# Kernel optimization log

Hardware: AMD Instinct MI355X
Metric: run time of the kernel (lower is better)

The kernel has to match this reference:

```python
import jax, jax.numpy as jnp
import numpy as np

# Mamba config (HF defaults for hidden_size=256)
VOCAB = 4096
H = 256          # hidden_size
I = 512          # intermediate_size = 2*H
N = 16           # state_size
R = 16           # time_step_rank = ceil(H/16)
K = 4            # conv_kernel
NUM_LAYERS = 4
B, L = 4, 1024
EPS = 1e-5


def _rmsnorm(x, w):
    return x * jax.lax.rsqrt(jnp.mean(x * x, axis=-1, keepdims=True) + EPS) * w


def setup_inputs() -> dict:
    key = jax.random.key(0)
    ks = jax.random.split(key, 20)
    s = 0.02
    Lyr = NUM_LAYERS
    inp = {
        'input_ids': jax.random.randint(ks[0], (B, L), 0, VOCAB),
        'lengths': jax.random.randint(ks[1], (B,), 1, L + 1),
        'embed': jax.random.normal(ks[2], (VOCAB, H)) * s,
        'norm_w': jnp.ones((Lyr, H)),
        'in_proj_w': jax.random.normal(ks[3], (Lyr, 2 * I, H)) * s,
        'conv_w': jax.random.normal(ks[4], (Lyr, I, K)) * s,
        'conv_b': jnp.zeros((Lyr, I)),
        'x_proj_w': jax.random.normal(ks[5], (Lyr, R + 2 * N, I)) * s,
        'dt_proj_w': jax.random.normal(ks[6], (Lyr, I, R)) * s,
        'dt_proj_b': jax.random.normal(ks[7], (Lyr, I)) * 0.5 - 4.0,
        'A_log': jnp.log(jnp.broadcast_to(jnp.arange(1, N + 1, dtype=jnp.float32), (Lyr, I, N))),
        'D': jnp.ones((Lyr, I)),
        'out_proj_w': jax.random.normal(ks[8], (Lyr, H, I)) * s,
        'final_norm_w': jnp.ones((H,)),
        'head_w1': jax.random.normal(ks[9], (H // 4, H)) * s,
        'head_b1': jnp.zeros((H // 4,)),
        'head_w2': jax.random.normal(ks[10], (1, H // 4)) * s,
        'head_b2': jnp.zeros((1,)),
    }
    return inp


def _mixer(x, in_proj_w, conv_w, conv_b, x_proj_w, dt_proj_w, dt_proj_b, A_log, D_, out_proj_w):
    b, l, _ = x.shape
    proj = x @ in_proj_w.T                      # (b,l,2I)
    xs, gate = proj[..., :I], proj[..., I:]
    # depthwise causal conv1d (kernel K, left pad K-1)
    xp = jnp.pad(xs, ((0, 0), (K - 1, 0), (0, 0)))
    conv = sum(xp[:, k:k + l, :] * conv_w[:, k] for k in range(K))
    xs = jax.nn.silu(conv + conv_b)             # (b,l,I)
    ssm = xs @ x_proj_w.T                       # (b,l,R+2N)
    dt_r, Bmat, Cmat = ssm[..., :R], ssm[..., R:R + N], ssm[..., R + N:]
    dt = jax.nn.softplus(dt_r @ dt_proj_w.T + dt_proj_b)   # (b,l,I)
    A = -jnp.exp(A_log)                         # (I,N)
    dA = jnp.exp(dt[..., None] * A)             # (b,l,I,N)
    dBu = (dt * xs)[..., None] * Bmat[:, :, None, :]        # (b,l,I,N)

    def step(state, inputs):
        a_t, bu_t, c_t = inputs                 # (b,I,N),(b,I,N),(b,N)
        state = a_t * state + bu_t
        y = jnp.einsum('bdn,bn->bd', state, c_t)
        return state, y

    state0 = jnp.zeros((b, I, N), dtype=x.dtype)
    _, ys = jax.lax.scan(step, state0, (dA.transpose(1, 0, 2, 3),
                                        dBu.transpose(1, 0, 2, 3),
                                        Cmat.transpose(1, 0, 2)))
    ys = ys.transpose(1, 0, 2)                  # (b,l,I)
    y = (ys + xs * D_) * jax.nn.silu(gate)
    return y @ out_proj_w.T                     # (b,l,H)


def reference(input_ids, lengths, embed, norm_w, in_proj_w, conv_w, conv_b,
              x_proj_w, dt_proj_w, dt_proj_b, A_log, D, out_proj_w,
              final_norm_w, head_w1, head_b1, head_w2, head_b2):
    h = embed[input_ids]                        # (B,L,H)
    for i in range(NUM_LAYERS):
        res = h
        x = _rmsnorm(h, norm_w[i])
        h = res + _mixer(x, in_proj_w[i], conv_w[i], conv_b[i], x_proj_w[i],
                         dt_proj_w[i], dt_proj_b[i], A_log[i], D[i], out_proj_w[i])
    h = _rmsnorm(h, final_norm_w)
    pooled = h[jnp.arange(h.shape[0]), lengths - 1]         # (B,H)
    hd = jax.nn.gelu(pooled @ head_w1.T + head_b1, approximate=False)
    out = hd @ head_w2.T + head_b2
    return out.squeeze(-1)                      # (B,)
```

## Files before the change

### kernel.cpp

```cpp
#include <hip/hip_runtime.h>
#include <hip/hip_bf16.h>

#define HDIM 256
#define IDIM 512
#define NST 16
#define KCONV 4
#define LAYERS 4
#define BATCH 4
#define LSEQ 1024
#define TOK (BATCH * LSEQ)

typedef unsigned short u16;
typedef float f32x4 __attribute__((ext_vector_type(4)));
typedef short bf16x8 __attribute__((ext_vector_type(8)));

static __device__ __forceinline__ u16 f2bf(float f) {
    __hip_bfloat16 h = __float2bfloat16(f);
    return reinterpret_cast<u16&>(h);
}
static __device__ __forceinline__ float bf2f(u16 b) {
    return __builtin_bit_cast(float, (unsigned)b << 16);
}
static __device__ __forceinline__ float bfup(uint2 u, int j) {
    unsigned w = (j < 2) ? u.x : u.y;
    unsigned bits = (j & 1) ? (w & 0xffff0000u) : (w << 16);
    return __builtin_bit_cast(float, bits);
}

#define DPP_ROW_ADD(p, CTRL)                                                   \
    p += __builtin_bit_cast(float, __builtin_amdgcn_update_dpp(                \
             0, __builtin_bit_cast(int, p), CTRL, 0xf, 0xf, false))

__global__ __launch_bounds__(256) void embed_kernel(const int* __restrict__ ids,
                                                    const float* __restrict__ embed,
                                                    float* __restrict__ h) {
    int idx = blockIdx.x * 256 + threadIdx.x;
    if (idx < TOK * HDIM) {
        int tok = idx >> 8;
        int c = idx & (HDIM - 1);
        h[idx] = embed[ids[tok] * HDIM + c];
    }
}

__global__ __launch_bounds__(256) void cvt4_bf16_kernel(const float* __restrict__ s0, u16* __restrict__ d0,
                                                        const float* __restrict__ s1, u16* __restrict__ d1,
                                                        const float* __restrict__ s2, u16* __restrict__ d2,
                                                        const float* __restrict__ s3, u16* __restrict__ d3) {
    const float* in;
    u16* out;
    int base;
    int bid = blockIdx.x;
    if (bid < 1024)      { in = s0; out = d0; base = bid; }
    else if (bid < 1536) { in = s1; out = d1; base = bid - 1024; }
    else if (bid < 1632) { in = s2; out = d2; base = bid - 1536; }
    else                 { in = s3; out = d3; base = bid - 1632; }
    int j = (base * 256 + threadIdx.x) * 4;
    float4 v = *(const float4*)&in[j];
    unsigned lo = (unsigned)f2bf(v.x) | ((unsigned)f2bf(v.y) << 16);
    unsigned hi = (unsigned)f2bf(v.z) | ((unsigned)f2bf(v.w) << 16);
    *(uint2*)&out[j] = make_uint2(lo, hi);
}

__global__ __launch_bounds__(256) void rmsnorm_kernel(const float* __restrict__ h,
                                                      const float* __restrict__ w,
                                                      u16* __restrict__ xb) {
    int wid = threadIdx.x >> 6, lane = threadIdx.x & 63;
    int tok = blockIdx.x * 4 + wid;
    float4 v = *(const float4*)&h[(size_t)tok * HDIM + lane * 4];
    float s = v.x * v.x + v.y * v.y + v.z * v.z + v.w * v.w;
    #pragma unroll
    for (int m = 32; m >= 1; m >>= 1) s += __shfl_xor(s, m, 64);
    float rstd = rsqrtf(s * (1.0f / HDIM) + 1e-5f);
    float4 wv = *(const float4*)&w[lane * 4];
    unsigned lo = (unsigned)f2bf(v.x * rstd * wv.x) | ((unsigned)f2bf(v.y * rstd * wv.y) << 16);
    unsigned hi = (unsigned)f2bf(v.z * rstd * wv.z) | ((unsigned)f2bf(v.w * rstd * wv.w) << 16);
    *(uint2*)&xb[(size_t)tok * HDIM + lane * 4] = make_uint2(lo, hi);
}

__global__ __launch_bounds__(256) void gemm_bf16_kernel(const u16* __restrict__ A,
                                                        const u16* __restrict__ W,
                                                        u16* __restrict__ C,
                                                        int M, int N, int K) {
    const int BM = 128, BK = 32;
    __shared__ __align__(16) u16 Al[BM][BK + 8];
    __shared__ __align__(16) u16 Bl[BM][BK + 8];
    int m0 = blockIdx.y * BM, n0 = blockIdx.x * BM;
    int tid = threadIdx.x;
    int lane = tid & 63;
    int wid = tid >> 6;
    int wr = wid >> 1, wc = wid & 1;
    int r = lane & 15, g = lane >> 4;

    f32x4 acc[4][4] = {};

    int srow = tid & 127;
    const u16* src = (tid < 128) ? (A + (size_t)(m0 + srow) * K)
                                 : (W + (size_t)(n0 + srow) * K);
    u16* dstrow = (tid < 128) ? &Al[srow][0] : &Bl[srow][0];

    for (int k0 = 0; k0 < K; k0 += BK) {
        uint4 v0 = *(const uint4*)(src + k0);
        uint4 v1 = *(const uint4*)(src + k0 + 8);
        uint4 v2 = *(const uint4*)(src + k0 + 16);
        uint4 v3 = *(const uint4*)(src + k0 + 24);
        __syncthreads();
        *(uint4*)(dstrow)      = v0;
        *(uint4*)(dstrow + 8)  = v1;
        *(uint4*)(dstrow + 16) = v2;
        *(uint4*)(dstrow + 24) = v3;
        __syncthreads();

        bf16x8 af[4], bfr[4];
        #pragma unroll
        for (int f = 0; f < 4; ++f) {
            af[f]  = *(const bf16x8*)&Al[wr * 64 + f * 16 + r][g * 8];
            bfr[f] = *(const bf16x8*)&Bl[wc * 64 + f * 16 + r][g * 8];
        }
        #pragma unroll
        for (int fm = 0; fm < 4; ++fm)
            #pragma unroll
            for (int fn = 0; fn < 4; ++fn)
                acc[fm][fn] = __builtin_amdgcn_mfma_f32_16x16x32_bf16(
                    af[fm], bfr[fn], acc[fm][fn], 0, 0, 0);
    }

    #pragma unroll
    for (int fm = 0; fm < 4; ++fm) {
        #pragma unroll
        for (int fn = 0; fn < 4; ++fn) {
            int col = n0 + wc * 64 + fn * 16 + r;
            #pragma unroll
            for (int v = 0; v < 4; ++v) {
                int row = m0 + wr * 64 + fm * 16 + g * 4 + v;
                C[(size_t)row * N + col] = f2bf(acc[fm][fn][v]);
            }
        }
    }
}

__global__ __launch_bounds__(256) void outproj_norm_kernel(const u16* __restrict__ Y,
                                                           const u16* __restrict__ W,
                                                           const float* __restrict__ nw,
                                                           float* __restrict__ h,
                                                           u16* __restrict__ xb) {
    __shared__ float sH[16][260];
    int m0 = blockIdx.x * 16;
    int tid = threadIdx.x;
    int lane = tid & 63;
    int w = tid >> 6;
    int r = lane & 15, g = lane >> 4;

    f32x4 acc[4] = {};
    const u16* yrow  = Y + (size_t)(m0 + r) * 512 + g * 8;
    const u16* wbase = W + (size_t)(w * 64 + r) * 512 + g * 8;
    #pragma unroll
    for (int k0 = 0; k0 < 512; k0 += 32) {
        bf16x8 af = *(const bf16x8*)(yrow + k0);
        #pragma unroll
        for (int fn = 0; fn < 4; ++fn) {
            bf16x8 bfr = *(const bf16x8*)(wbase + (size_t)fn * 16 * 512 + k0);
            acc[fn] = __builtin_amdgcn_mfma_f32_16x16x32_bf16(af, bfr, acc[fn], 0, 0, 0);
        }
    }

    #pragma unroll
    for (int fn = 0; fn < 4; ++fn) {
        int col = w * 64 + fn * 16 + r;
        #pragma unroll
        for (int v = 0; v < 4; ++v) {
            int row = g * 4 + v;
            size_t off = (size_t)(m0 + row) * HDIM + col;
            float hv = h[off] + acc[fn][v];
            h[off] = hv;
            sH[row][col] = hv;
        }
    }
    __syncthreads();

    int row = tid >> 4, part = tid & 15;
    const float* sr = &sH[row][part * 16];
    float s = 0.f;
    #pragma unroll
    for (int j = 0; j < 16; ++j) s = fmaf(sr[j], sr[j], s);
    DPP_ROW_ADD(s, 0xB1);
    DPP_ROW_ADD(s, 0x4E);
    DPP_ROW_ADD(s, 0x141);
    DPP_ROW_ADD(s, 0x140);
    float rstd = rsqrtf(s * (1.0f / HDIM) + 1e-5f);
    const float* nwp = &nw[part * 16];
    unsigned pk[8];
    #pragma unroll
    for (int j = 0; j < 8; ++j) {
        u16 lo = f2bf(sr[2 * j]     * rstd * nwp[2 * j]);
        u16 hi = f2bf(sr[2 * j + 1] * rstd * nwp[2 * j + 1]);
        pk[j] = (unsigned)lo | ((unsigned)hi << 16);
    }
    u16* dst = xb + (size_t)(m0 + row) * HDIM + part * 16;
    *(uint4*)(dst)     = make_uint4(pk[0], pk[1], pk[2], pk[3]);
    *(uint4*)(dst + 8) = make_uint4(pk[4], pk[5], pk[6], pk[7]);
}

__global__ __launch_bounds__(512) void xproj_kernel(const u16* __restrict__ proj,
                                                    const float* __restrict__ cw,
                                                    const float* __restrict__ cb,
                                                    const u16* __restrict__ W,
                                                    const u16* __restrict__ dtw,
                                                    const float* __restrict__ dtb,
                                                    float* __restrict__ bc,
                                                    float* __restrict__ dtT,
                                                    u16* __restrict__ xs_T,
                                                    u16* __restrict__ gate_T) {
    __shared__ __align__(16) u16 xsL[16][520];
    __shared__ float sP[8][16][52];
    __shared__ float sT[16][52];
    int m0 = blockIdx.x * 16;
    int tid = threadIdx.x;
    int lane = tid & 63;
    int w = tid >> 6;
    int r = lane & 15, g = lane >> 4;
    int tl = m0 & (LSEQ - 1);

    {
        int ic = tid;
        const u16* pxs = proj + (size_t)m0 * 1024 + ic;
        float4 wq = *(const float4*)&cw[ic * 4];
        float bias = cb[ic];
        float a0 = (tl >= 3) ? bf2f(pxs[-3 * 1024]) : 0.f;
        float a1 = (tl >= 2) ? bf2f(pxs[-2 * 1024]) : 0.f;
        float a2 = (tl >= 1) ? bf2f(pxs[-1 * 1024]) : 0.f;
        unsigned xr[8], gr[8];
        #pragma unroll
        for (int t = 0; t < 16; ++t) {
            float a3 = bf2f(pxs[t * 1024]);
            float acc = bias;
            acc = fmaf(a0, wq.x, acc);
            acc = fmaf(a1, wq.y, acc);
            acc = fmaf(a2, wq.z, acc);
            acc = fmaf(a3, wq.w, acc);
            float xsv = acc / (1.f + __expf(-acc));
            u16 xb16 = f2bf(xsv);
            xsL[t][ic] = xb16;
            float gv = bf2f(pxs[t * 1024 + 512]);
            gv = gv / (1.f + __expf(-gv));
            u16 gb16 = f2bf(gv);
            if (t & 1) { xr[t >> 1] |= (unsigned)xb16 << 16; gr[t >> 1] |= (unsigned)gb16 << 16; }
            else       { xr[t >> 1] = xb16;                   gr[t >> 1] = gb16; }
            a0 = a1; a1 = a2; a2 = a3;
        }
        size_t trow = (size_t)ic * TOK + m0;
        *(uint4*)&xs_T[trow]       = make_uint4(xr[0], xr[1], xr[2], xr[3]);
        *(uint4*)&xs_T[trow + 8]   = make_uint4(xr[4], xr[5], xr[6], xr[7]);
        *(uint4*)&gate_T[trow]     = make_uint4(gr[0], gr[1], gr[2], gr[3]);
        *(uint4*)&gate_T[trow + 8] = make_uint4(gr[4], gr[5], gr[6], gr[7]);
    }
    __syncthreads();

    {
        f32x4 acc[3] = {};
        const u16* wbase = W + (size_t)r * 512 + w * 64 + g * 8;
        #pragma unroll
        for (int ks = 0; ks < 2; ++ks) {
            bf16x8 af = *(const bf16x8*)&xsL[r][w * 64 + ks * 32 + g * 8];
            #pragma unroll
            for (int fn = 0; fn < 3; ++fn) {
                bf16x8 bfr = *(const bf16x8*)(wbase + (size_t)fn * 16 * 512 + ks * 32);
                acc[fn] = __builtin_amdgcn_mfma_f32_16x16x32_bf16(af, bfr, acc[fn], 0, 0, 0);
            }
        }
        #pragma unroll
        for (int fn = 0; fn < 3; ++fn)
            #pragma unroll
            for (int v = 0; v < 4; ++v)
                sP[w][g * 4 + v][fn * 16 + r] = acc[fn][v];
    }
    __syncthreads();

    #pragma unroll
    for (int e = 0; e < 2; ++e) {
        int o = tid + e * 512;
        if (o < 768) {
            int row = o / 48, col = o - row * 48;
            float s = 0.f;
            #pragma unroll
            for (int p = 0; p < 8; ++p) s += sP[p][row][col];
            sT[row][col] = s;
        }
    }
    __syncthreads();

    {
        int l = tid;
        int group = l >> 7;
        int rem = l & 127;
        int side = rem >> 6;
        int nn = (rem >> 2) & 15;
        int tq = rem & 3;
        bc[(size_t)blockIdx.x * 512 + l] = sT[group * 4 + tq][16 + side * 16 + nn];
    }

    bf16x8 bv = {};
    if (g < 2) {
        #pragma unroll
        for (int j = 0; j < 8; ++j)
            bv[j] = (short)f2bf(sT[r][g * 8 + j]);
    }
    int mbase = w * 64;
    #pragma unroll
    for (int mf = 0; mf < 4; ++mf) {
        int mrow = mbase + mf * 16;
        bf16x8 av = {};
        if (g < 2) av = *(const bf16x8*)(dtw + (size_t)(mrow + r) * 16 + g * 8);
        f32x4 a2 = __builtin_amdgcn_mfma_f32_16x16x32_bf16(av, bv, f32x4{}, 0, 0, 0);
        float4 b4 = *(const float4*)&dtb[mrow + g * 4];
        #pragma unroll
        for (int v = 0; v < 4; ++v) {
            int i = mrow + g * 4 + v;
            float val = a2[v] + (&b4.x)[v];
            val = fmaxf(val, 0.f) + log1pf(__expf(-fabsf(val)));
            dtT[(size_t)i * TOK + m0 + r] = val;
        }
    }
}

__global__ __launch_bounds__(256, 4) void scan_kernel(const float* __restrict__ dt_T,
                                                      const u16* __restrict__ xs_T,
                                                      const u16* __restrict__ gate_T,
                                                      const float* __restrict__ bc,
                                                      const float* __restrict__ A_log,
                                                      const float* __restrict__ Dw,
                                                      u16* __restrict__ yb) {
    const int NC = 16;
    int n = threadIdx.x & 15;
    int c = threadIdx.x >> 4;

    int lin = (blockIdx.x & 7) * 256 + (blockIdx.x >> 3);
    int b = lin >> 9;
    int i = lin & (IDIM - 1);

    float A = -__expf(A_log[i * NST + n]);

    __shared__ float aprodS[NC][17];
    __shared__ float stendS[NC][17];
    __shared__ float incS[NC][17];

    int t0 = c * 64;
    size_t coff = (size_t)i * TOK + b * LSEQ + t0;
    const float4* dtp = (const float4*)(dt_T + coff);
    const uint2*  xsp = (const uint2*)(xs_T + coff);
    const u16*    xg  = xs_T + coff;
    const u16*    gg  = gate_T + coff;
    const float4* bp  = (const float4*)(bc + (size_t)(b * LSEQ + t0) * 32);

    float aprod = 1.f, st = 0.f;
    #pragma unroll
    for (int q = 0; q < 16; ++q) {
        float4 d4 = dtp[q];
        uint2  xu = xsp[q];
        float4 B4 = __builtin_bit_cast(float4, bp[q * 32 + n]);
        #pragma unroll
        for (int j = 0; j < 4; ++j) {
            float dtv = (&d4.x)[j];
            float dA  = __expf(dtv * A);
            aprod *= dA;
            st = fmaf(dA, st, dtv * bfup(xu, j) * (&B4.x)[j]);
        }
    }
    aprodS[c][n] = aprod;
    stendS[c][n] = st;
    __syncthreads();

    if (threadIdx.x < 16) {
        int nn = threadIdx.x;
        float carry = 0.f;
        for (int cc = 0; cc < NC; ++cc) {
            incS[cc][nn] = carry;
            carry = fmaf(aprodS[cc][nn], carry, stendS[cc][nn]);
        }
    }
    __syncthreads();

    st = incS[c][n];
    float Dv = Dw[i];
    u16* y_b = yb + ((size_t)b * LSEQ + t0) * IDIM + i;
    float yacc = 0.f;

    #pragma unroll 8
    for (int q = 0; q < 16; ++q) {
        float4 d4 = dtp[q];
        uint2  xu = xsp[q];
        float4 B4 = __builtin_bit_cast(float4, bp[q * 32 + n]);
        float4 C4 = __builtin_bit_cast(float4, bp[q * 32 + 16 + n]);
        #pragma unroll
        for (int j = 0; j < 4; ++j) {
            float dtv = (&d4.x)[j];
            float xv  = bfup(xu, j);
            float dA  = __expf(dtv * A);
            st = fmaf(dA, st, dtv * xv * (&B4.x)[j]);
            float py = st * (&C4.x)[j];
            DPP_ROW_ADD(py, 0xB1);
            DPP_ROW_ADD(py, 0x4E);
            DPP_ROW_ADD(py, 0x141);
            DPP_ROW_ADD(py, 0x140);
            yacc = (((q & 3) * 4 + j) == n) ? py : yacc;
        }
        if ((q & 3) == 3) {
            int base = (q - 3) * 4;
            float xvn = bf2f(xg[base + n]);
            float gvn = bf2f(gg[base + n]);
            float yv = fmaf(xvn, Dv, yacc) * gvn;
            y_b[(size_t)(base + n) * IDIM] = f2bf(yv);
        }
    }
}

__global__ __launch_bounds__(256) void head_kernel(const float* __restrict__ h,
                                                   const int* __restrict__ lengths,
                                                   const float* __restrict__ fw,
                                                   const float* __restrict__ w1,
                                                   const float* __restrict__ b1,
                                                   const float* __restrict__ w2,
                                                   const float* __restrict__ b2,
                                                   float* __restrict__ out) {
    int b = blockIdx.x;
    int c = threadIdx.x;
    int len = lengths[b];
    const float* row = h + ((size_t)b * LSEQ + (len - 1)) * HDIM;
    float v = row[c];
    float s = v * v;
    #pragma unroll
    for (int m = 32; m >= 1; m >>= 1) s += __shfl_xor(s, m, 64);
    __shared__ float ls[4];
    __shared__ float pooled[HDIM];
    __shared__ float hd[64];
    if ((c & 63) == 0) ls[c >> 6] = s;
    __syncthreads();
    float tot = ls[0] + ls[1] + ls[2] + ls[3];
    float rstd = rsqrtf(tot * (1.0f / HDIM) + 1e-5f);
    pooled[c] = v * rstd * fw[c];
    __syncthreads();
    if (c < 64) {
        float a = b1[c];
        for (int k = 0; k < HDIM; ++k) a = fmaf(pooled[k], w1[c * HDIM + k], a);
        float g = 0.5f * a * (1.f + erff(a * 0.70710678118654752f));
        hd[c] = g * w2[c];
    }
    __syncthreads();
    if (c == 0) {
        float o = b2[0];
        for (int k = 0; k < 64; ++k) o += hd[k];
        out[b] = o;
    }
}

extern "C" void kernel_launch(void* const* d_in, const int* in_sizes, int n_in,
                              void* d_out, int out_size, void* d_ws, size_t ws_size,
                              hipStream_t stream) {
    const int*   ids         = (const int*)d_in[0];
    const int*   lengths     = (const int*)d_in[1];
    const float* embed       = (const float*)d_in[2];
    const float* norm_w      = (const float*)d_in[3];
    const float* in_proj_w   = (const float*)d_in[4];
    const float* conv_w      = (const float*)d_in[5];
    const float* conv_b      = (const float*)d_in[6];
    const float* x_proj_w    = (const float*)d_in[7];
    const float* dt_proj_w   = (const float*)d_in[8];
    const float* dt_proj_b   = (const float*)d_in[9];
    const float* A_log       = (const float*)d_in[10];
    const float* Dw          = (const float*)d_in[11];
    const float* out_proj_w  = (const float*)d_in[12];
    const float* final_norm_w= (const float*)d_in[13];
    const float* head_w1     = (const float*)d_in[14];
    const float* head_b1     = (const float*)d_in[15];
    const float* head_w2     = (const float*)d_in[16];
    const float* head_b2     = (const float*)d_in[17];

    float* ws   = (float*)d_ws;
    float* h    = ws;
    float* dtT  = h    + 1048576;
    float* bc   = dtT  + 2097152;
    u16* xb   = (u16*)(bc + 131072);
    u16* yb   = xb   + 1048576;
    u16* wib  = yb   + 2097152;
    u16* wob  = wib  + 1048576;
    u16* xwb  = wob  + 524288;
    u16* dtwb = xwb  + 98304;
    u16* projb= dtwb + 32768;
    u16* xsT  = projb+ 4194304;
    u16* gT   = xsT  + 2097152;

    embed_kernel<<<TOK * HDIM / 256, 256, 0, stream>>>(ids, embed, h);
    cvt4_bf16_kernel<<<1664, 256, 0, stream>>>(in_proj_w, wib, out_proj_w, wob,
                                               x_proj_w, xwb, dt_proj_w, dtwb);
    rmsnorm_kernel<<<TOK / 4, 256, 0, stream>>>(h, norm_w, xb);

    for (int l = 0; l < LAYERS; ++l) {
        gemm_bf16_kernel<<<dim3(1024 / 128, TOK / 128), 256, 0, stream>>>(
            xb, wib + (size_t)l * 2 * IDIM * HDIM, projb, TOK, 2 * IDIM, HDIM);
        xproj_kernel<<<TOK / 16, 512, 0, stream>>>(
            projb, conv_w + l * IDIM * KCONV, conv_b + l * IDIM,
            xwb + (size_t)l * 48 * IDIM, dtwb + (size_t)l * IDIM * 16,
            dt_proj_b + l * IDIM, bc, dtT, xsT, gT);
        scan_kernel<<<BATCH * IDIM, 256, 0, stream>>>(
            dtT, xsT, gT, bc, A_log + (size_t)l * IDIM * NST, Dw + l * IDIM, yb);
        const float* nw_next = (l + 1 < LAYERS) ? (norm_w + (l + 1) * HDIM) : final_norm_w;
        outproj_norm_kernel<<<TOK / 16, 256, 0, stream>>>(
            yb, wob + (size_t)l * HDIM * IDIM, nw_next, h, xb);
    }

    head_kernel<<<BATCH, 256, 0, stream>>>(h, lengths, final_norm_w,
                                           head_w1, head_b1, head_w2, head_b2,
                                           (float*)d_out);
}
```

Baseline: 314.9 us.

## Scan four state channels per thread and pack four (batch,channel) pairs per block

Result: slower. 323.4 us (+2.7%).

```diff
diff --git a/kernel.cpp b/kernel.cpp
--- a/kernel.cpp
+++ b/kernel.cpp
@@ -322,26 +322,32 @@
     }
 }
 
-__global__ __launch_bounds__(256, 4) void scan_kernel(const float* __restrict__ dt_T,
-                                                      const u16* __restrict__ xs_T,
-                                                      const u16* __restrict__ gate_T,
-                                                      const float* __restrict__ bc,
-                                                      const float* __restrict__ A_log,
-                                                      const float* __restrict__ Dw,
-                                                      u16* __restrict__ yb) {
-    const int NC = 16;
-    int n = threadIdx.x & 15;
-    int c = threadIdx.x >> 4;
-
-    int lin = (blockIdx.x & 7) * 256 + (blockIdx.x >> 3);
-    int b = lin >> 9;
-    int i = lin & (IDIM - 1);
-
-    float A = -__expf(A_log[i * NST + n]);
-
-    __shared__ float aprodS[NC][17];
-    __shared__ float stendS[NC][17];
-    __shared__ float incS[NC][17];
+__global__ __launch_bounds__(256) void scan_kernel(const float* __restrict__ dt_T,
+                                                   const u16* __restrict__ xs_T,
+                                                   const u16* __restrict__ gate_T,
+                                                   const float* __restrict__ bc,
+                                                   const float* __restrict__ A_log,
+                                                   const float* __restrict__ Dw,
+                                                   u16* __restrict__ yb) {
+    int tid = threadIdx.x;
+    int w = tid >> 6;
+    int lane = tid & 63;
+    int nq = lane & 3;
+    int c = lane >> 2;
+
+    int lin = (blockIdx.x & 7) * 64 + (blockIdx.x >> 3);
+    int base = lin * 4;
+    int bi = base + w;
+    int b = bi >> 9;
+    int i = bi & (IDIM - 1);
+
+    float A[4];
+    #pragma unroll
+    for (int k = 0; k < 4; ++k) A[k] = -__expf(A_log[i * NST + nq * 4 + k]);
+
+    __shared__ float aprodS[4][16][16];
+    __shared__ float stendS[4][16][16];
+    __shared__ float incS[4][16][16];
 
     int t0 = c * 64;
     size_t coff = (size_t)i * TOK + b * LSEQ + t0;
@@ -351,65 +357,76 @@
     const u16*    gg  = gate_T + coff;
     const float4* bp  = (const float4*)(bc + (size_t)(b * LSEQ + t0) * 32);
 
-    float aprod = 1.f, st = 0.f;
+    float st[4] = {0.f, 0.f, 0.f, 0.f};
+    float sumdt = 0.f;
     #pragma unroll
     for (int q = 0; q < 16; ++q) {
         float4 d4 = dtp[q];
         uint2  xu = xsp[q];
-        float4 B4 = __builtin_bit_cast(float4, bp[q * 32 + n]);
+        float4 Bq[4];
+        #pragma unroll
+        for (int k = 0; k < 4; ++k) Bq[k] = __builtin_bit_cast(float4, bp[q * 32 + nq * 4 + k]);
         #pragma unroll
         for (int j = 0; j < 4; ++j) {
             float dtv = (&d4.x)[j];
-            float dA  = __expf(dtv * A);
-            aprod *= dA;
-            st = fmaf(dA, st, dtv * bfup(xu, j) * (&B4.x)[j]);
-        }
-    }
-    aprodS[c][n] = aprod;
-    stendS[c][n] = st;
-    __syncthreads();
-
-    if (threadIdx.x < 16) {
-        int nn = threadIdx.x;
+            sumdt += dtv;
+            float dxv = dtv * bfup(xu, j);
+            #pragma unroll
+            for (int k = 0; k < 4; ++k)
+                st[k] = fmaf(__expf(dtv * A[k]), st[k], dxv * (&Bq[k].x)[j]);
+        }
+    }
+    #pragma unroll
+    for (int k = 0; k < 4; ++k) {
+        aprodS[w][c][nq * 4 + k] = __expf(A[k] * sumdt);
+        stendS[w][c][nq * 4 + k] = st[k];
+    }
+    __syncthreads();
+
+    if (tid < 64) {
+        int ch = tid >> 4, n = tid & 15;
         float carry = 0.f;
-        for (int cc = 0; cc < NC; ++cc) {
-            incS[cc][nn] = carry;
-            carry = fmaf(aprodS[cc][nn], carry, stendS[cc][nn]);
-        }
-    }
-    __syncthreads();
-
-    st = incS[c][n];
+        for (int cc = 0; cc < 16; ++cc) {
+            incS[ch][cc][n] = carry;
+            carry = fmaf(aprodS[ch][cc][n], carry, stendS[ch][cc][n]);
+        }
+    }
+    __syncthreads();
+
+    #pragma unroll
+    for (int k = 0; k < 4; ++k) st[k] = incS[w][c][nq * 4 + k];
     float Dv = Dw[i];
     u16* y_b = yb + ((size_t)b * LSEQ + t0) * IDIM + i;
-    float yacc = 0.f;
-
-    #pragma unroll 8
+
+    #pragma unroll
     for (int q = 0; q < 16; ++q) {
         float4 d4 = dtp[q];
         uint2  xu = xsp[q];
-        float4 B4 = __builtin_bit_cast(float4, bp[q * 32 + n]);
-        float4 C4 = __builtin_bit_cast(float4, bp[q * 32 + 16 + n]);
+        float4 Bq[4], Cq[4];
+        #pragma unroll
+        for (int k = 0; k < 4; ++k) {
+            Bq[k] = __builtin_bit_cast(float4, bp[q * 32 + nq * 4 + k]);
+            Cq[k] = __builtin_bit_cast(float4, bp[q * 32 + 16 + nq * 4 + k]);
+        }
+        float yacc = 0.f;
         #pragma unroll
         for (int j = 0; j < 4; ++j) {
             float dtv = (&d4.x)[j];
-            float xv  = bfup(xu, j);
-            float dA  = __expf(dtv * A);
-            st = fmaf(dA, st, dtv * xv * (&B4.x)[j]);
-            float py = st * (&C4.x)[j];
+            float dxv = dtv * bfup(xu, j);
+            float py = 0.f;
+            #pragma unroll
+            for (int k = 0; k < 4; ++k) {
+                st[k] = fmaf(__expf(dtv * A[k]), st[k], dxv * (&Bq[k].x)[j]);
+                py = fmaf(st[k], (&Cq[k].x)[j], py);
+            }
             DPP_ROW_ADD(py, 0xB1);
             DPP_ROW_ADD(py, 0x4E);
-            DPP_ROW_ADD(py, 0x141);
-            DPP_ROW_ADD(py, 0x140);
-            yacc = (((q & 3) * 4 + j) == n) ? py : yacc;
-        }
-        if ((q & 3) == 3) {
-            int base = (q - 3) * 4;
-            float xvn = bf2f(xg[base + n]);
-            float gvn = bf2f(gg[base + n]);
-            float yv = fmaf(xvn, Dv, yacc) * gvn;
-            y_b[(size_t)(base + n) * IDIM] = f2bf(yv);
-        }
+            yacc = (j == nq) ? py : yacc;
+        }
+        int t = q * 4 + nq;
+        float xvn = bf2f(xg[t]);
+        float gvn = bf2f(gg[t]);
+        y_b[(size_t)t * IDIM] = f2bf(fmaf(xvn, Dv, yacc) * gvn);
     }
 }
 
@@ -500,7 +517,7 @@
             projb, conv_w + l * IDIM * KCONV, conv_b + l * IDIM,
             xwb + (size_t)l * 48 * IDIM, dtwb + (size_t)l * IDIM * 16,
             dt_proj_b + l * IDIM, bc, dtT, xsT, gT);
-        scan_kernel<<<BATCH * IDIM, 256, 0, stream>>>(
+        scan_kernel<<<BATCH * IDIM / 4, 256, 0, stream>>>(
             dtT, xsT, gT, bc, A_log + (size_t)l * IDIM * NST, Dw + l * IDIM, yb);
         const float* nw_next = (l + 1 < LAYERS) ? (norm_w + (l + 1) * HDIM) : final_norm_w;
         outproj_norm_kernel<<<TOK / 16, 256, 0, stream>>>(
```
